# Optimization experiments

Measured on AMD Instinct MI355X. Metric: run time of the kernel, lower is better.

## Reference

```python
import jax, jax.numpy as jnp
import numpy as np

B, N, C = 4, 2048, 1024
HEADS, DHEAD = 16, 64
EPS = 1e-7
SCALE = DHEAD ** (-0.5)


def setup_inputs() -> dict:
    key = jax.random.key(0)
    k1, k2, k3, k4 = jax.random.split(key, 4)
    inner = HEADS * DHEAD
    return {
        "x": jax.random.normal(k1, (B, N, C), dtype=jnp.float32),
        "gamma": jnp.ones((1, 1, C), dtype=jnp.float32),
        "Wq": jax.random.normal(k2, (inner, C), dtype=jnp.float32) * np.sqrt(1.0 / C),
        "Wkv": jax.random.normal(k3, (2 * DHEAD, C), dtype=jnp.float32) * np.sqrt(1.0 / C),
        "Wo": jax.random.normal(k4, (C, inner), dtype=jnp.float32) * np.sqrt(1.0 / inner) * 1e-5,
        "ls_scale": jnp.full((C,), 1e-4, dtype=jnp.float32),
    }


def reference(x, gamma, Wq, Wkv, Wo, ls_scale):
    # BiasFreeLayerNorm: divide by unbiased std (no mean subtraction), scale by gamma
    std = jnp.std(x, axis=-1, ddof=1, keepdims=True)
    xn = (x / (std + EPS)) * gamma
    # q from normalized x, k/v from the ORIGINAL x (kv_input = x before norm)
    q = xn @ Wq.T                       # [B, N, H*D]
    kv = x @ Wkv.T                      # [B, N, 2*D]
    k, v = kv[..., :DHEAD], kv[..., DHEAD:]  # shared single kv head (MQA)
    q = q.reshape(B, N, HEADS, DHEAD).transpose(0, 2, 1, 3) * SCALE  # [B, H, N, D]
    sim = jnp.einsum('bhid,bjd->bhij', q, k)
    attn = jax.nn.softmax(sim, axis=-1)
    out = jnp.einsum('bhij,bjd->bhid', attn, v)       # [B, H, N, D]
    out = out.transpose(0, 2, 1, 3).reshape(B, N, HEADS * DHEAD)
    out = out @ Wo.T
    return ls_scale * out
```

## Files before the change

### kernel.cpp

```cpp
#include <hip/hip_runtime.h>
#include <hip/hip_bf16.h>
#include <stdint.h>

typedef __attribute__((ext_vector_type(8))) short short8;
typedef __attribute__((ext_vector_type(4))) float f32x4;
typedef __attribute__((ext_vector_type(16))) float f32x16;
typedef __attribute__((ext_vector_type(4))) unsigned short us4;

#define B_ 4
#define N_ 2048
#define C_ 1024
#define H_ 16
#define D_ 64

__device__ __forceinline__ unsigned short f2bf(float f) {
  union { float f; unsigned u; } v; v.f = f;
  unsigned u = v.u;
  u += 0x7fffu + ((u >> 16) & 1u);
  return (unsigned short)(u >> 16);
}

__device__ __forceinline__ unsigned short bfc(float f) {
  union { __hip_bfloat16 h; unsigned short u; } v;
  v.h = __float2bfloat16(f);
  return v.u;
}

__device__ __forceinline__ unsigned pk2(float lo, float hi) {
  return ((unsigned)bfc(hi) << 16) | (unsigned)bfc(lo);
}

__device__ __forceinline__ void pswap(unsigned& a, unsigned& b) {
  asm("v_permlane32_swap_b32 %0, %1" : "+v"(a), "+v"(b));
}

__device__ __forceinline__ void glds16(const unsigned short* g, const unsigned short* l) {
  __builtin_amdgcn_global_load_lds(
      (const __attribute__((address_space(1))) void*)(uintptr_t)g,
      (__attribute__((address_space(3))) void*)(uintptr_t)l, 16, 0, 0);
}

__device__ __forceinline__ f32x4 mfma16(short8 a, short8 b, f32x4 c) {
  return __builtin_amdgcn_mfma_f32_16x16x32_bf16(a, b, c, 0, 0, 0);
}

__device__ __forceinline__ f32x16 mfma32(short8 a, short8 b, f32x16 c) {
  return __builtin_amdgcn_mfma_f32_32x32x16_bf16(a, b, c, 0, 0, 0);
}

__global__ __launch_bounds__(256) void prep_cast_k(const float* __restrict__ x,
                                                   const float* __restrict__ gamma,
                                                   unsigned short* __restrict__ xb,
                                                   float* __restrict__ rstd_v,
                                                   const float* __restrict__ wq,
                                                   const float* __restrict__ wkv,
                                                   const float* __restrict__ wo,
                                                   unsigned short* __restrict__ dq,
                                                   unsigned short* __restrict__ dkv,
                                                   unsigned short* __restrict__ dwo) {
  const int t = threadIdx.x;
  if (blockIdx.x >= 8192) {
    const int i = (blockIdx.x - 8192) * 256 + t;
    if (i < 262144) {
      const float4 v = ((const float4*)wq)[i];
      const float4 gv = ((const float4*)gamma)[i & 255];
      us4 o;
      o.x = f2bf(v.x * gv.x); o.y = f2bf(v.y * gv.y);
      o.z = f2bf(v.z * gv.z); o.w = f2bf(v.w * gv.w);
      ((us4*)dq)[i] = o;
    } else {
      const float* s;
      unsigned short* d;
      int j;
      if (i < 294912) { s = wkv; d = dkv; j = i - 262144; }
      else { s = wo; d = dwo; j = i - 294912; }
      const float4 v = ((const float4*)s)[j];
      us4 o; o.x = f2bf(v.x); o.y = f2bf(v.y); o.z = f2bf(v.z); o.w = f2bf(v.w);
      ((us4*)d)[j] = o;
    }
    return;
  }
  const int row = blockIdx.x;
  const float4 v = ((const float4*)(x + (size_t)row * C_))[t];
  float s1 = v.x + v.y + v.z + v.w;
  float s2 = v.x * v.x + v.y * v.y + v.z * v.z + v.w * v.w;
#pragma unroll
  for (int off = 32; off > 0; off >>= 1) {
    s1 += __shfl_down(s1, off);
    s2 += __shfl_down(s2, off);
  }
  __shared__ float r1[4], r2[4];
  if ((t & 63) == 0) { r1[t >> 6] = s1; r2[t >> 6] = s2; }
  __syncthreads();
  s1 = r1[0] + r1[1] + r1[2] + r1[3];
  s2 = r2[0] + r2[1] + r2[2] + r2[3];
  const float var = (s2 - s1 * s1 * (1.0f / C_)) * (1.0f / (C_ - 1));
  const float rstd = 1.0f / (sqrtf(var) + 1e-7f);
  if (t == 0) rstd_v[row] = rstd;
  us4 a;
  a.x = f2bf(v.x); a.y = f2bf(v.y); a.z = f2bf(v.z); a.w = f2bf(v.w);
  ((us4*)(xb + (size_t)row * C_))[t] = a;
}

__global__ __launch_bounds__(256, 2) void qkv_gemm(const unsigned short* __restrict__ xb,
                                                   const unsigned short* __restrict__ wq,
                                                   const unsigned short* __restrict__ wkv,
                                                   const float* __restrict__ rstd_v,
                                                   unsigned short* __restrict__ qo,
                                                   unsigned short* __restrict__ kvo,
                                                   unsigned short* __restrict__ vtb) {
  const bool iskv = (blockIdx.x == 8);
  const unsigned short* Bw = iskv ? wkv : wq;
  const int n0 = iskv ? 0 : blockIdx.x * 128;
  const int K = 1024, m0 = blockIdx.y * 128;

  __shared__ unsigned short At[128 * 32];
  __shared__ unsigned short Bt[128 * 32];
  const int t = threadIdx.x;
  const int w = t >> 6, l = t & 63;
  const int ql = l & 15, g = l >> 4;
  const int wr = (w >> 1) * 64, wc = (w & 1) * 64;

  const int pr0 = t >> 2, pb0 = t & 3;
  const int lb0 = pb0 ^ ((pr0 >> 1) & 3);
  const int pr1 = 64 + (t >> 2);
  const int lb1 = pb0 ^ ((pr1 >> 1) & 3);
  const unsigned short* Ab = xb + (size_t)m0 * K;
  const unsigned short* Bb = Bw + (size_t)n0 * K;

  f32x4 acc[4][4];
#pragma unroll
  for (int i = 0; i < 4; ++i)
#pragma unroll
    for (int j = 0; j < 4; ++j) acc[i][j] = f32x4{0.f, 0.f, 0.f, 0.f};

  for (int k0 = 0; k0 < K; k0 += 32) {
    glds16(Ab + (size_t)pr0 * K + k0 + lb0 * 8, &At[w * 512]);
    glds16(Ab + (size_t)pr1 * K + k0 + lb1 * 8, &At[2048 + w * 512]);
    glds16(Bb + (size_t)pr0 * K + k0 + lb0 * 8, &Bt[w * 512]);
    glds16(Bb + (size_t)pr1 * K + k0 + lb1 * 8, &Bt[2048 + w * 512]);
    __syncthreads();
    short8 af[4], bfr[4];
#pragma unroll
    for (int i = 0; i < 4; ++i) {
      const int row = wr + i * 16 + ql;
      af[i] = *(const short8*)&At[row * 32 + ((g ^ ((row >> 1) & 3)) * 8)];
    }
#pragma unroll
    for (int i = 0; i < 4; ++i) {
      const int row = wc + i * 16 + ql;
      bfr[i] = *(const short8*)&Bt[row * 32 + ((g ^ ((row >> 1) & 3)) * 8)];
    }
#pragma unroll
    for (int mi = 0; mi < 4; ++mi)
#pragma unroll
      for (int ni = 0; ni < 4; ++ni)
        acc[mi][ni] = mfma16(af[mi], bfr[ni], acc[mi][ni]);
    __syncthreads();
  }

  if (!iskv) {
    float rs[4][4];
#pragma unroll
    for (int mi = 0; mi < 4; ++mi)
#pragma unroll
      for (int r = 0; r < 4; ++r)
        rs[mi][r] = 0.18033688011112042f * rstd_v[m0 + wr + mi * 16 + g * 4 + r];
#pragma unroll
    for (int mi = 0; mi < 4; ++mi)
#pragma unroll
      for (int ni = 0; ni < 4; ++ni) {
        const int col = n0 + wc + ni * 16 + ql;
#pragma unroll
        for (int r = 0; r < 4; ++r) {
          const int row = m0 + wr + mi * 16 + g * 4 + r;
          qo[(size_t)row * 1024 + col] = f2bf(acc[mi][ni][r] * rs[mi][r]);
        }
      }
  } else if (wc == 0) {
#pragma unroll
    for (int mi = 0; mi < 4; ++mi)
#pragma unroll
      for (int ni = 0; ni < 4; ++ni) {
        const int col = ni * 16 + ql;
#pragma unroll
        for (int r = 0; r < 4; ++r) {
          const int row = m0 + wr + mi * 16 + g * 4 + r;
          kvo[(size_t)row * 128 + col] = f2bf(acc[mi][ni][r]);
        }
      }
  } else {
    const int brow = m0 >> 11;
    unsigned short* vb = vtb + (size_t)brow * 64 * 2048;
#pragma unroll
    for (int mi = 0; mi < 4; ++mi) {
      const int nbase = (m0 & 2047) + wr + mi * 16 + g * 4;
#pragma unroll
      for (int ni = 0; ni < 4; ++ni) {
        const int d = ni * 16 + ql;
        us4 st;
        st.x = f2bf(acc[mi][ni][0]);
        st.y = f2bf(acc[mi][ni][1]);
        st.z = f2bf(acc[mi][ni][2]);
        st.w = f2bf(acc[mi][ni][3]);
        *(us4*)&vb[(size_t)d * 2048 + nbase] = st;
      }
    }
  }
}

__global__ __launch_bounds__(256, 2) void gemm_o(const unsigned short* __restrict__ A,
                                                 const unsigned short* __restrict__ Bw,
                                                 float* __restrict__ Cout,
                                                 const float* __restrict__ colscale,
                                                 int M, int N, int K) {
  __shared__ unsigned short At[128 * 32];
  __shared__ unsigned short Bt[128 * 32];
  const int t = threadIdx.x;
  const int w = t >> 6, l = t & 63;
  const int ql = l & 15, g = l >> 4;
  const int wr = (w >> 1) * 64, wc = (w & 1) * 64;
  const int m0 = blockIdx.y * 128, n0 = blockIdx.x * 128;

  const int pr0 = t >> 2, pb0 = t & 3;
  const int lb0 = pb0 ^ ((pr0 >> 1) & 3);
  const int pr1 = 64 + (t >> 2);
  const int lb1 = pb0 ^ ((pr1 >> 1) & 3);
  const unsigned short* Ab = A + (size_t)m0 * K;
  const unsigned short* Bb = Bw + (size_t)n0 * K;

  f32x4 acc[4][4];
#pragma unroll
  for (int i = 0; i < 4; ++i)
#pragma unroll
    for (int j = 0; j < 4; ++j) acc[i][j] = f32x4{0.f, 0.f, 0.f, 0.f};

  for (int k0 = 0; k0 < K; k0 += 32) {
    glds16(Ab + (size_t)pr0 * K + k0 + lb0 * 8, &At[w * 512]);
    glds16(Ab + (size_t)pr1 * K + k0 + lb1 * 8, &At[2048 + w * 512]);
    glds16(Bb + (size_t)pr0 * K + k0 + lb0 * 8, &Bt[w * 512]);
    glds16(Bb + (size_t)pr1 * K + k0 + lb1 * 8, &Bt[2048 + w * 512]);
    __syncthreads();
    short8 af[4], bfr[4];
#pragma unroll
    for (int i = 0; i < 4; ++i) {
      const int row = wr + i * 16 + ql;
      af[i] = *(const short8*)&At[row * 32 + ((g ^ ((row >> 1) & 3)) * 8)];
    }
#pragma unroll
    for (int i = 0; i < 4; ++i) {
      const int row = wc + i * 16 + ql;
      bfr[i] = *(const short8*)&Bt[row * 32 + ((g ^ ((row >> 1) & 3)) * 8)];
    }
#pragma unroll
    for (int mi = 0; mi < 4; ++mi)
#pragma unroll
      for (int ni = 0; ni < 4; ++ni)
        acc[mi][ni] = mfma16(af[mi], bfr[ni], acc[mi][ni]);
    __syncthreads();
  }

#pragma unroll
  for (int mi = 0; mi < 4; ++mi)
#pragma unroll
    for (int ni = 0; ni < 4; ++ni) {
      const int col = n0 + wc + ni * 16 + ql;
      const float cs = colscale[col];
#pragma unroll
      for (int r = 0; r < 4; ++r) {
        const int row = m0 + wr + mi * 16 + g * 4 + r;
        Cout[(size_t)row * N + col] = acc[mi][ni][r] * cs;
      }
    }
}

__global__ __launch_bounds__(256, 3) void attn_k(const unsigned short* __restrict__ qb,
                                                 const unsigned short* __restrict__ kvb,
                                                 const unsigned short* __restrict__ vtb,
                                                 unsigned short* __restrict__ ao) {
  __shared__ unsigned short Kt[2][64 * 64];
  __shared__ unsigned short Vt[2][64 * 64];

  const int idx = blockIdx.x;
  const int qc = idx & 15, hd = (idx >> 4) & 15, b = idx >> 8;
  const int t = threadIdx.x, w = t >> 6, l = t & 63;
  const int l31 = l & 31, hi = l >> 5, sw = l & 7;
  const int q0 = qc * 128 + w * 32;

  const unsigned short* qrow = qb + (size_t)(b * N_ + q0 + l31) * C_ + hd * D_;
  short8 Qf[4];
#pragma unroll
  for (int ks = 0; ks < 4; ++ks)
    Qf[ks] = *(const short8*)(qrow + 16 * ks + 8 * hi);

  const unsigned short* kvrow = kvb + (size_t)(b * N_) * 128;
  const unsigned short* vtrow = vtb + (size_t)b * 64 * 2048;
  const int sr = l >> 3;
  const int blk = ((l & 7) ^ sr) << 3;
  const int row0 = 16 * w + sr;
  const int row1 = row0 + 8;

  auto stage = [&](int bi, int kt) {
    glds16(kvrow + (size_t)(kt * 64 + row0) * 128 + blk, &Kt[bi][(2 * w) * 512]);
    glds16(kvrow + (size_t)(kt * 64 + row1) * 128 + blk, &Kt[bi][(2 * w + 1) * 512]);
    glds16(vtrow + (size_t)row0 * 2048 + kt * 64 + blk, &Vt[bi][(2 * w) * 512]);
    glds16(vtrow + (size_t)row1 * 2048 + kt * 64 + blk, &Vt[bi][(2 * w + 1) * 512]);
  };

  f32x16 o[2];
#pragma unroll
  for (int dh = 0; dh < 2; ++dh)
#pragma unroll
    for (int r = 0; r < 16; ++r) o[dh][r] = 0.f;
  float lsum = 0.f;

  auto tilec = [&](int bi) {
    short8 Pf[4];
#pragma unroll
    for (int half = 0; half < 2; ++half) {
      const int kro = (32 * half + l31) * 64;
      short8 Kf[4];
#pragma unroll
      for (int ks = 0; ks < 4; ++ks)
        Kf[ks] = *(const short8*)&Kt[bi][kro + (((2 * ks + hi) ^ sw) << 3)];
      f32x16 s;
#pragma unroll
      for (int r = 0; r < 16; ++r) s[r] = 0.f;
#pragma unroll
      for (int ks = 0; ks < 4; ++ks) s = mfma32(Kf[ks], Qf[ks], s);
#pragma unroll
      for (int w2 = 0; w2 < 2; ++w2) {
        const float p0 = __builtin_amdgcn_exp2f(s[8 * w2 + 0]);
        const float p1 = __builtin_amdgcn_exp2f(s[8 * w2 + 1]);
        const float p2 = __builtin_amdgcn_exp2f(s[8 * w2 + 2]);
        const float p3 = __builtin_amdgcn_exp2f(s[8 * w2 + 3]);
        const float p4 = __builtin_amdgcn_exp2f(s[8 * w2 + 4]);
        const float p5 = __builtin_amdgcn_exp2f(s[8 * w2 + 5]);
        const float p6 = __builtin_amdgcn_exp2f(s[8 * w2 + 6]);
        const float p7 = __builtin_amdgcn_exp2f(s[8 * w2 + 7]);
        lsum += ((p0 + p1) + (p2 + p3)) + ((p4 + p5) + (p6 + p7));
        unsigned a0 = pk2(p0, p1), a1 = pk2(p2, p3);
        unsigned b0 = pk2(p4, p5), b1 = pk2(p6, p7);
        pswap(a0, b0);
        pswap(a1, b1);
        union { unsigned u[4]; short8 v; } cv;
        cv.u[0] = a0; cv.u[1] = a1; cv.u[2] = b0; cv.u[3] = b1;
        Pf[2 * half + w2] = cv.v;
      }
    }

    __builtin_amdgcn_s_setprio(1);
#pragma unroll
    for (int dh = 0; dh < 2; ++dh) {
      const int vro = (32 * dh + l31) * 64;
      short8 Vf[4];
#pragma unroll
      for (int win = 0; win < 4; ++win)
        Vf[win] = *(const short8*)&Vt[bi][vro + (((2 * win + hi) ^ sw) << 3)];
#pragma unroll
      for (int win = 0; win < 4; ++win)
        o[dh] = mfma32(Vf[win], Pf[win], o[dh]);
    }
    __builtin_amdgcn_s_setprio(0);
  };

  stage(0, 0);
  for (int kt = 0; kt < 32; kt += 2) {
    __syncthreads();
    stage(1, kt + 1);
    tilec(0);
    __syncthreads();
    if (kt + 2 < 32) stage(0, kt + 2);
    tilec(1);
  }

  lsum += __shfl_xor(lsum, 32);
  const float inv = 1.0f / lsum;

  unsigned short* orow = ao + (size_t)(b * N_ + q0 + l31) * C_ + hd * D_;
#pragma unroll
  for (int dh = 0; dh < 2; ++dh)
#pragma unroll
    for (int r2 = 0; r2 < 4; ++r2) {
      us4 st;
      st.x = bfc(o[dh][4 * r2 + 0] * inv);
      st.y = bfc(o[dh][4 * r2 + 1] * inv);
      st.z = bfc(o[dh][4 * r2 + 2] * inv);
      st.w = bfc(o[dh][4 * r2 + 3] * inv);
      *(us4*)(orow + 32 * dh + 8 * r2 + 4 * hi) = st;
    }
}

extern "C" void kernel_launch(void* const* d_in, const int* in_sizes, int n_in,
                              void* d_out, int out_size, void* d_ws, size_t ws_size,
                              hipStream_t stream) {
  const float* x = (const float*)d_in[0];
  const float* gamma = (const float*)d_in[1];
  const float* Wq = (const float*)d_in[2];
  const float* Wkv = (const float*)d_in[3];
  const float* Wo = (const float*)d_in[4];
  const float* ls = (const float*)d_in[5];
  float* out = (float*)d_out;

  unsigned short* ws = (unsigned short*)d_ws;
  const size_t R = (size_t)B_ * N_;
  unsigned short* xb = ws;
  unsigned short* qbuf = xb + R * C_;
  unsigned short* kvb = qbuf + R * C_;
  unsigned short* aob = kvb + R * 128;
  unsigned short* wqb = aob + R * C_;
  unsigned short* wkvb = wqb + (size_t)C_ * C_;
  unsigned short* wob = wkvb + (size_t)128 * C_;
  unsigned short* vtb = wob + (size_t)C_ * C_;
  float* rstd = (float*)(vtb + (size_t)4 * 64 * 2048);

  prep_cast_k<<<(int)R + 2176, 256, 0, stream>>>(x, gamma, xb, rstd,
                                                 Wq, Wkv, Wo, wqb, wkvb, wob);
  qkv_gemm<<<dim3(9, R / 128), 256, 0, stream>>>(xb, wqb, wkvb, rstd,
                                                 qbuf, kvb, vtb);
  attn_k<<<B_ * H_ * (N_ / 128), 256, 0, stream>>>(qbuf, kvb, vtb, aob);
  gemm_o<<<dim3(C_ / 128, R / 128), 256, 0, stream>>>(aob, wob, out, ls,
                                                      (int)R, C_, C_);
}
```

Before: 161.0 us.

## Process two heads per attention block to reuse shared K/V tiles

Each attention workgroup now handles two query heads against the shared MQA K/V stream, which halves the grid size and the number of K/V tile loads into LDS and reuses each K and V fragment for two MFMA chains. It doubles per-thread accumulator and Q register state and lowers launch bounds to 2 waves per SIMD. The risks are lower occupancy and fewer blocks (512) for latency hiding on a large GPU.

```diff
diff --git a/kernel.cpp b/kernel.cpp
--- a/kernel.cpp
+++ b/kernel.cpp
@@ -274,7 +274,7 @@
     }
 }
 
-__global__ __launch_bounds__(256, 3) void attn_k(const unsigned short* __restrict__ qb,
+__global__ __launch_bounds__(256, 2) void attn_k(const unsigned short* __restrict__ qb,
                                                  const unsigned short* __restrict__ kvb,
                                                  const unsigned short* __restrict__ vtb,
                                                  unsigned short* __restrict__ ao) {
@@ -282,16 +282,18 @@
   __shared__ unsigned short Vt[2][64 * 64];
 
   const int idx = blockIdx.x;
-  const int qc = idx & 15, hd = (idx >> 4) & 15, b = idx >> 8;
+  const int qc = idx & 15, hp = (idx >> 4) & 7, b = idx >> 7;
   const int t = threadIdx.x, w = t >> 6, l = t & 63;
   const int l31 = l & 31, hi = l >> 5, sw = l & 7;
   const int q0 = qc * 128 + w * 32;
 
-  const unsigned short* qrow = qb + (size_t)(b * N_ + q0 + l31) * C_ + hd * D_;
-  short8 Qf[4];
-#pragma unroll
-  for (int ks = 0; ks < 4; ++ks)
-    Qf[ks] = *(const short8*)(qrow + 16 * ks + 8 * hi);
+  const unsigned short* qrow = qb + (size_t)(b * N_ + q0 + l31) * C_ + hp * 128;
+  short8 Qf[2][4];
+#pragma unroll
+  for (int h = 0; h < 2; ++h)
+#pragma unroll
+    for (int ks = 0; ks < 4; ++ks)
+      Qf[h][ks] = *(const short8*)(qrow + 64 * h + 16 * ks + 8 * hi);
 
   const unsigned short* kvrow = kvb + (size_t)(b * N_) * 128;
   const unsigned short* vtrow = vtb + (size_t)b * 64 * 2048;
@@ -307,15 +309,17 @@
     glds16(vtrow + (size_t)row1 * 2048 + kt * 64 + blk, &Vt[bi][(2 * w + 1) * 512]);
   };
 
-  f32x16 o[2];
-#pragma unroll
-  for (int dh = 0; dh < 2; ++dh)
-#pragma unroll
-    for (int r = 0; r < 16; ++r) o[dh][r] = 0.f;
-  float lsum = 0.f;
+  f32x16 o[2][2];
+#pragma unroll
+  for (int h = 0; h < 2; ++h)
+#pragma unroll
+    for (int dh = 0; dh < 2; ++dh)
+#pragma unroll
+      for (int r = 0; r < 16; ++r) o[h][dh][r] = 0.f;
+  float lsum[2] = {0.f, 0.f};
 
   auto tilec = [&](int bi) {
-    short8 Pf[4];
+    short8 Pf[2][4];
 #pragma unroll
     for (int half = 0; half < 2; ++half) {
       const int kro = (32 * half + l31) * 64;
@@ -323,29 +327,35 @@
 #pragma unroll
       for (int ks = 0; ks < 4; ++ks)
         Kf[ks] = *(const short8*)&Kt[bi][kro + (((2 * ks + hi) ^ sw) << 3)];
-      f32x16 s;
-#pragma unroll
-      for (int r = 0; r < 16; ++r) s[r] = 0.f;
-#pragma unroll
-      for (int ks = 0; ks < 4; ++ks) s = mfma32(Kf[ks], Qf[ks], s);
-#pragma unroll
-      for (int w2 = 0; w2 < 2; ++w2) {
-        const float p0 = __builtin_amdgcn_exp2f(s[8 * w2 + 0]);
-        const float p1 = __builtin_amdgcn_exp2f(s[8 * w2 + 1]);
-        const float p2 = __builtin_amdgcn_exp2f(s[8 * w2 + 2]);
-        const float p3 = __builtin_amdgcn_exp2f(s[8 * w2 + 3]);
-        const float p4 = __builtin_amdgcn_exp2f(s[8 * w2 + 4]);
-        const float p5 = __builtin_amdgcn_exp2f(s[8 * w2 + 5]);
-        const float p6 = __builtin_amdgcn_exp2f(s[8 * w2 + 6]);
-        const float p7 = __builtin_amdgcn_exp2f(s[8 * w2 + 7]);
-        lsum += ((p0 + p1) + (p2 + p3)) + ((p4 + p5) + (p6 + p7));
-        unsigned a0 = pk2(p0, p1), a1 = pk2(p2, p3);
-        unsigned b0 = pk2(p4, p5), b1 = pk2(p6, p7);
-        pswap(a0, b0);
-        pswap(a1, b1);
-        union { unsigned u[4]; short8 v; } cv;
-        cv.u[0] = a0; cv.u[1] = a1; cv.u[2] = b0; cv.u[3] = b1;
-        Pf[2 * half + w2] = cv.v;
+      f32x16 sA, sB;
+#pragma unroll
+      for (int r = 0; r < 16; ++r) { sA[r] = 0.f; sB[r] = 0.f; }
+#pragma unroll
+      for (int ks = 0; ks < 4; ++ks) sA = mfma32(Kf[ks], Qf[0][ks], sA);
+#pragma unroll
+      for (int ks = 0; ks < 4; ++ks) sB = mfma32(Kf[ks], Qf[1][ks], sB);
+#pragma unroll
+      for (int h = 0; h < 2; ++h) {
+        const f32x16& s = h ? sB : sA;
+#pragma unroll
+        for (int w2 = 0; w2 < 2; ++w2) {
+          const float p0 = __builtin_amdgcn_exp2f(s[8 * w2 + 0]);
+          const float p1 = __builtin_amdgcn_exp2f(s[8 * w2 + 1]);
+          const float p2 = __builtin_amdgcn_exp2f(s[8 * w2 + 2]);
+          const float p3 = __builtin_amdgcn_exp2f(s[8 * w2 + 3]);
+          const float p4 = __builtin_amdgcn_exp2f(s[8 * w2 + 4]);
+          const float p5 = __builtin_amdgcn_exp2f(s[8 * w2 + 5]);
+          const float p6 = __builtin_amdgcn_exp2f(s[8 * w2 + 6]);
+          const float p7 = __builtin_amdgcn_exp2f(s[8 * w2 + 7]);
+          lsum[h] += ((p0 + p1) + (p2 + p3)) + ((p4 + p5) + (p6 + p7));
+          unsigned a0 = pk2(p0, p1), a1 = pk2(p2, p3);
+          unsigned b0 = pk2(p4, p5), b1 = pk2(p6, p7);
+          pswap(a0, b0);
+          pswap(a1, b1);
+          union { unsigned u[4]; short8 v; } cv;
+          cv.u[0] = a0; cv.u[1] = a1; cv.u[2] = b0; cv.u[3] = b1;
+          Pf[h][2 * half + w2] = cv.v;
+        }
       }
     }
 
@@ -359,7 +369,10 @@
         Vf[win] = *(const short8*)&Vt[bi][vro + (((2 * win + hi) ^ sw) << 3)];
 #pragma unroll
       for (int win = 0; win < 4; ++win)
-        o[dh] = mfma32(Vf[win], Pf[win], o[dh]);
+        o[0][dh] = mfma32(Vf[win], Pf[0][win], o[0][dh]);
+#pragma unroll
+      for (int win = 0; win < 4; ++win)
+        o[1][dh] = mfma32(Vf[win], Pf[1][win], o[1][dh]);
     }
     __builtin_amdgcn_s_setprio(0);
   };
@@ -374,21 +387,24 @@
     tilec(1);
   }
 
-  lsum += __shfl_xor(lsum, 32);
-  const float inv = 1.0f / lsum;
-
-  unsigned short* orow = ao + (size_t)(b * N_ + q0 + l31) * C_ + hd * D_;
-#pragma unroll
-  for (int dh = 0; dh < 2; ++dh)
-#pragma unroll
-    for (int r2 = 0; r2 < 4; ++r2) {
-      us4 st;
-      st.x = bfc(o[dh][4 * r2 + 0] * inv);
-      st.y = bfc(o[dh][4 * r2 + 1] * inv);
-      st.z = bfc(o[dh][4 * r2 + 2] * inv);
-      st.w = bfc(o[dh][4 * r2 + 3] * inv);
-      *(us4*)(orow + 32 * dh + 8 * r2 + 4 * hi) = st;
-    }
+#pragma unroll
+  for (int h = 0; h < 2; ++h) {
+    lsum[h] += __shfl_xor(lsum[h], 32);
+    const float inv = 1.0f / lsum[h];
+    unsigned short* orow =
+        ao + (size_t)(b * N_ + q0 + l31) * C_ + hp * 128 + 64 * h;
+#pragma unroll
+    for (int dh = 0; dh < 2; ++dh)
+#pragma unroll
+      for (int r2 = 0; r2 < 4; ++r2) {
+        us4 st;
+        st.x = bfc(o[h][dh][4 * r2 + 0] * inv);
+        st.y = bfc(o[h][dh][4 * r2 + 1] * inv);
+        st.z = bfc(o[h][dh][4 * r2 + 2] * inv);
+        st.w = bfc(o[h][dh][4 * r2 + 3] * inv);
+        *(us4*)(orow + 32 * dh + 8 * r2 + 4 * hi) = st;
+      }
+  }
 }
 
 extern "C" void kernel_launch(void* const* d_in, const int* in_sizes, int n_in,
@@ -418,7 +434,7 @@
                                                  Wq, Wkv, Wo, wqb, wkvb, wob);
   qkv_gemm<<<dim3(9, R / 128), 256, 0, stream>>>(xb, wqb, wkvb, rstd,
                                                  qbuf, kvb, vtb);
-  attn_k<<<B_ * H_ * (N_ / 128), 256, 0, stream>>>(qbuf, kvb, vtb, aob);
+  attn_k<<<B_ * (H_ / 2) * (N_ / 128), 256, 0, stream>>>(qbuf, kvb, vtb, aob);
   gemm_o<<<dim3(C_ / 128, R / 128), 256, 0, stream>>>(aob, wob, out, ls,
                                                       (int)R, C_, C_);
 }
```

Result: faster. 154.9 us (-3.8%).
